# Performance work log

Measured on AMD Instinct MI355X. Metric: run time of the kernel, lower is better.

## Reference

```python
import jax, jax.numpy as jnp
import numpy as np

NUM_KNOTS = 64
HEAD_DIM = 4
SCALE = 0.5  # 1/sqrt(4)


def setup_inputs() -> dict:
    key = jax.random.key(0)
    ks = jax.random.split(key, 6)
    B, L, D = 4, 128, 256
    s = 1.0 / np.sqrt(D)
    return {
        "x": jax.random.normal(ks[0], (B, L, D), dtype=jnp.float32),
        "Wq": jax.random.normal(ks[1], (D, D), dtype=jnp.float32) * s,
        "Wk": jax.random.normal(ks[2], (D, D), dtype=jnp.float32) * s,
        "Wv": jax.random.normal(ks[3], (D, D), dtype=jnp.float32) * s,
        "Wo": jax.random.normal(ks[4], (D, D), dtype=jnp.float32) * s,
        "bo": jnp.zeros((D,), dtype=jnp.float32),
    }


def reference(x, Wq, Wk, Wv, Wo, bo):
    # x: [B, L, D], D = NUM_KNOTS * HEAD_DIM = 256
    B, L, D = x.shape
    N = L * NUM_KNOTS  # flattened 'knot' sequence length
    # nn.Linear applies x @ W.T
    q = (x @ Wq.T).reshape(B, N, HEAD_DIM)
    k = (x @ Wk.T).reshape(B, N, HEAD_DIM)
    v = (x @ Wv.T).reshape(B, N, HEAD_DIM)
    # full attention over the length-N knot sequence (head_dim = 4)
    logits = jnp.einsum("bnd,bmd->bnm", q, k) * SCALE  # [B, N, N]
    attn = jax.nn.softmax(logits, axis=-1)
    out = jnp.einsum("bnm,bmd->bnd", attn, v).reshape(B, L, D)
    return out @ Wo.T + bo
```

## Files before the change

### kernel.cpp

```cpp
#include <hip/hip_runtime.h>

#define NQ 8192
#define BLROWS 512
#define DIM 256

#define QSCALE 0.7213475204444817f

typedef float v2f __attribute__((ext_vector_type(2)));

__device__ __forceinline__ float ex2(float x) {
#if __has_builtin(__builtin_amdgcn_exp2f)
    return __builtin_amdgcn_exp2f(x);
#else
    return exp2f(x);
#endif
}

__device__ __forceinline__ void proj4_body(
    const float* __restrict__ A, const float* __restrict__ W,
    const float* __restrict__ bias, float* __restrict__ C,
    float scale, int rb)
{
    const int j = threadIdx.x;
    float acc[4] = {0.f, 0.f, 0.f, 0.f};
    const float4* __restrict__ W4 = reinterpret_cast<const float4*>(W + j * DIM);
    const float*  __restrict__ A0 = A + rb * DIM;

    #pragma unroll 4
    for (int d4 = 0; d4 < DIM / 4; ++d4) {
        const float4 w = W4[d4];
        #pragma unroll
        for (int r = 0; r < 4; ++r) {
            const float4 a = reinterpret_cast<const float4*>(A0 + r * DIM)[d4];
            acc[r] = fmaf(a.x, w.x, acc[r]);
            acc[r] = fmaf(a.y, w.y, acc[r]);
            acc[r] = fmaf(a.z, w.z, acc[r]);
            acc[r] = fmaf(a.w, w.w, acc[r]);
        }
    }
    const float b = bias ? bias[j] : 0.f;
    #pragma unroll
    for (int r = 0; r < 4; ++r)
        C[(rb + r) * DIM + j] = fmaf(acc[r], scale, b);
}

__global__ __launch_bounds__(256) void qkv_proj(
    const float* __restrict__ x,
    const float* __restrict__ Wq, const float* __restrict__ Wk,
    const float* __restrict__ Wv,
    float* __restrict__ Qb, float* __restrict__ Kb, float* __restrict__ Vb)
{
    const int m = blockIdx.y;
    const float* W = (m == 0) ? Wq : (m == 1) ? Wk : Wv;
    float* C       = (m == 0) ? Qb : (m == 1) ? Kb : Vb;
    const float sc = (m == 0) ? QSCALE : 1.0f;
    proj4_body(x, W, nullptr, C, sc, blockIdx.x * 4);
}

__global__ __launch_bounds__(256) void proj4_kernel(
    const float* __restrict__ A, const float* __restrict__ W,
    const float* __restrict__ bias, float* __restrict__ C, float scale)
{
    proj4_body(A, W, bias, C, scale, blockIdx.x * 4);
}

__global__ __launch_bounds__(256) void attn_partial(
    const float* __restrict__ Q, const float* __restrict__ K,
    const float* __restrict__ V, float* __restrict__ P)
{
    const int lane = threadIdx.x & 63;
    const int w    = __builtin_amdgcn_readfirstlane(threadIdx.x >> 6);
    const int qt   = blockIdx.x;
    const int ks   = blockIdx.y;
    const int b    = blockIdx.z;

    const float4* __restrict__ Qp = reinterpret_cast<const float4*>(Q) + b * NQ + qt * 256;
    const float4* __restrict__ Kp = reinterpret_cast<const float4*>(K) + b * NQ + ks * 1024 + w * 256;
    const float4* __restrict__ Vp = reinterpret_cast<const float4*>(V) + b * NQ + ks * 1024 + w * 256;

    v2f qx[2], qy[2], qz[2], qw[2];
    #pragma unroll
    for (int p = 0; p < 2; ++p) {
        const float4 t0 = Qp[(2 * p)     * 64 + lane];
        const float4 t1 = Qp[(2 * p + 1) * 64 + lane];
        qx[p] = v2f{t0.x, t1.x};
        qy[p] = v2f{t0.y, t1.y};
        qz[p] = v2f{t0.z, t1.z};
        qw[p] = v2f{t0.w, t1.w};
    }
    v2f a0[2], a1[2], a2[2], a3[2], ls[2];
    #pragma unroll
    for (int p = 0; p < 2; ++p) {
        a0[p] = v2f{0.f, 0.f}; a1[p] = v2f{0.f, 0.f};
        a2[p] = v2f{0.f, 0.f}; a3[p] = v2f{0.f, 0.f};
        ls[p] = v2f{0.f, 0.f};
    }

    #pragma unroll 8
    for (int j = 0; j < 256; ++j) {
        const float4 k4 = Kp[j];
        const float4 v4 = Vp[j];
        #pragma unroll
        for (int p = 0; p < 2; ++p) {
            v2f s = qx[p] * k4.x;
            s = __builtin_elementwise_fma(qy[p], v2f{k4.y, k4.y}, s);
            s = __builtin_elementwise_fma(qz[p], v2f{k4.z, k4.z}, s);
            s = __builtin_elementwise_fma(qw[p], v2f{k4.w, k4.w}, s);
            const v2f e = v2f{ex2(s[0]), ex2(s[1])};
            ls[p] += e;
            a0[p] = __builtin_elementwise_fma(e, v2f{v4.x, v4.x}, a0[p]);
            a1[p] = __builtin_elementwise_fma(e, v2f{v4.y, v4.y}, a1[p]);
            a2[p] = __builtin_elementwise_fma(e, v2f{v4.z, v4.z}, a2[p]);
            a3[p] = __builtin_elementwise_fma(e, v2f{v4.w, v4.w}, a3[p]);
        }
    }

    __shared__ float red[4][256][5];
    #pragma unroll
    for (int p = 0; p < 2; ++p) {
        #pragma unroll
        for (int e = 0; e < 2; ++e) {
            float* pr = &red[w][(2 * p + e) * 64 + lane][0];
            pr[0] = ls[p][e]; pr[1] = a0[p][e]; pr[2] = a1[p][e];
            pr[3] = a2[p][e]; pr[4] = a3[p][e];
        }
    }
    __syncthreads();

    float* __restrict__ Pb = P + (size_t)((b * 8 + ks) * 5) * NQ + qt * 256;
    const int qq = threadIdx.x;
    #pragma unroll
    for (int c = 0; c < 5; ++c) {
        const float sred = red[0][qq][c] + red[1][qq][c] + red[2][qq][c] + red[3][qq][c];
        Pb[c * NQ + qq] = sred;
    }
}

__global__ __launch_bounds__(256) void attn_merge(
    const float* __restrict__ P, float* __restrict__ AO)
{
    const int idx = blockIdx.x * 256 + threadIdx.x;
    const int b = idx >> 13;
    const int n = idx & (NQ - 1);
    float l = 0.f, x0 = 0.f, x1 = 0.f, x2 = 0.f, x3 = 0.f;
    #pragma unroll
    for (int s = 0; s < 8; ++s) {
        const float* Pb = P + (size_t)((b * 8 + s) * 5) * NQ + n;
        l  += Pb[0];
        x0 += Pb[NQ];
        x1 += Pb[2 * NQ];
        x2 += Pb[3 * NQ];
        x3 += Pb[4 * NQ];
    }
    const float inv = 1.0f / l;
    reinterpret_cast<float4*>(AO)[idx] = make_float4(x0 * inv, x1 * inv, x2 * inv, x3 * inv);
}

extern "C" void kernel_launch(void* const* d_in, const int* in_sizes, int n_in,
                              void* d_out, int out_size, void* d_ws, size_t ws_size,
                              hipStream_t stream) {
    const float* x  = (const float*)d_in[0];
    const float* Wq = (const float*)d_in[1];
    const float* Wk = (const float*)d_in[2];
    const float* Wv = (const float*)d_in[3];
    const float* Wo = (const float*)d_in[4];
    const float* bo = (const float*)d_in[5];
    float* out = (float*)d_out;

    float* Qb = (float*)d_ws;
    float* Kb = Qb + BLROWS * DIM;
    float* Vb = Kb + BLROWS * DIM;
    float* AO = Vb + BLROWS * DIM;
    float* P  = AO + BLROWS * DIM;

    qkv_proj<<<dim3(128, 3), 256, 0, stream>>>(x, Wq, Wk, Wv, Qb, Kb, Vb);
    attn_partial<<<dim3(32, 8, 4), 256, 0, stream>>>(Qb, Kb, Vb, P);
    attn_merge<<<128, 256, 0, stream>>>(P, AO);
    proj4_kernel<<<128, 256, 0, stream>>>(AO, Wo, bo, out, 1.0f);
}
```

Baseline: 91.94 us.

## Double key-split slices and fuse softmax merge into output projection

```diff
diff --git a/kernel.cpp b/kernel.cpp
--- a/kernel.cpp
+++ b/kernel.cpp
@@ -3,6 +3,7 @@
 #define NQ 8192
 #define BLROWS 512
 #define DIM 256
+#define KSLICES 16
 
 #define QSCALE 0.7213475204444817f
 
@@ -16,15 +17,22 @@
 #endif
 }
 
-__device__ __forceinline__ void proj4_body(
-    const float* __restrict__ A, const float* __restrict__ W,
-    const float* __restrict__ bias, float* __restrict__ C,
-    float scale, int rb)
+__global__ __launch_bounds__(256) void qkv_proj(
+    const float* __restrict__ x,
+    const float* __restrict__ Wq, const float* __restrict__ Wk,
+    const float* __restrict__ Wv,
+    float* __restrict__ Qb, float* __restrict__ Kb, float* __restrict__ Vb)
 {
-    const int j = threadIdx.x;
+    const int m = blockIdx.y;
+    const float* W = (m == 0) ? Wq : (m == 1) ? Wk : Wv;
+    float* C       = (m == 0) ? Qb : (m == 1) ? Kb : Vb;
+    const float sc = (m == 0) ? QSCALE : 1.0f;
+    const int j  = threadIdx.x;
+    const int rb = blockIdx.x * 4;
+
     float acc[4] = {0.f, 0.f, 0.f, 0.f};
     const float4* __restrict__ W4 = reinterpret_cast<const float4*>(W + j * DIM);
-    const float*  __restrict__ A0 = A + rb * DIM;
+    const float*  __restrict__ A0 = x + rb * DIM;
 
     #pragma unroll 4
     for (int d4 = 0; d4 < DIM / 4; ++d4) {
@@ -38,30 +46,9 @@
             acc[r] = fmaf(a.w, w.w, acc[r]);
         }
     }
-    const float b = bias ? bias[j] : 0.f;
     #pragma unroll
     for (int r = 0; r < 4; ++r)
-        C[(rb + r) * DIM + j] = fmaf(acc[r], scale, b);
-}
-
-__global__ __launch_bounds__(256) void qkv_proj(
-    const float* __restrict__ x,
-    const float* __restrict__ Wq, const float* __restrict__ Wk,
-    const float* __restrict__ Wv,
-    float* __restrict__ Qb, float* __restrict__ Kb, float* __restrict__ Vb)
-{
-    const int m = blockIdx.y;
-    const float* W = (m == 0) ? Wq : (m == 1) ? Wk : Wv;
-    float* C       = (m == 0) ? Qb : (m == 1) ? Kb : Vb;
-    const float sc = (m == 0) ? QSCALE : 1.0f;
-    proj4_body(x, W, nullptr, C, sc, blockIdx.x * 4);
-}
-
-__global__ __launch_bounds__(256) void proj4_kernel(
-    const float* __restrict__ A, const float* __restrict__ W,
-    const float* __restrict__ bias, float* __restrict__ C, float scale)
-{
-    proj4_body(A, W, bias, C, scale, blockIdx.x * 4);
+        C[(rb + r) * DIM + j] = acc[r] * sc;
 }
 
 __global__ __launch_bounds__(256) void attn_partial(
@@ -75,8 +62,8 @@
     const int b    = blockIdx.z;
 
     const float4* __restrict__ Qp = reinterpret_cast<const float4*>(Q) + b * NQ + qt * 256;
-    const float4* __restrict__ Kp = reinterpret_cast<const float4*>(K) + b * NQ + ks * 1024 + w * 256;
-    const float4* __restrict__ Vp = reinterpret_cast<const float4*>(V) + b * NQ + ks * 1024 + w * 256;
+    const float4* __restrict__ Kp = reinterpret_cast<const float4*>(K) + b * NQ + ks * 512 + w * 128;
+    const float4* __restrict__ Vp = reinterpret_cast<const float4*>(V) + b * NQ + ks * 512 + w * 128;
 
     v2f qx[2], qy[2], qz[2], qw[2];
     #pragma unroll
@@ -97,7 +84,7 @@
     }
 
     #pragma unroll 8
-    for (int j = 0; j < 256; ++j) {
+    for (int j = 0; j < 128; ++j) {
         const float4 k4 = Kp[j];
         const float4 v4 = Vp[j];
         #pragma unroll
@@ -127,7 +114,7 @@
     }
     __syncthreads();
 
-    float* __restrict__ Pb = P + (size_t)((b * 8 + ks) * 5) * NQ + qt * 256;
+    float* __restrict__ Pb = P + (size_t)((b * KSLICES + ks) * 5) * NQ + qt * 256;
     const int qq = threadIdx.x;
     #pragma unroll
     for (int c = 0; c < 5; ++c) {
@@ -136,24 +123,55 @@
     }
 }
 
-__global__ __launch_bounds__(256) void attn_merge(
-    const float* __restrict__ P, float* __restrict__ AO)
+__global__ __launch_bounds__(256) void merge_oproj(
+    const float* __restrict__ P, const float* __restrict__ Wo,
+    const float* __restrict__ bo, float* __restrict__ out)
 {
-    const int idx = blockIdx.x * 256 + threadIdx.x;
-    const int b = idx >> 13;
-    const int n = idx & (NQ - 1);
-    float l = 0.f, x0 = 0.f, x1 = 0.f, x2 = 0.f, x3 = 0.f;
+    __shared__ float aoL[4][DIM];
+
+    const int rb = blockIdx.x * 4;
+    const int b  = rb >> 7;
+    const int n0 = (rb & 127) * 64;
+    const int t  = threadIdx.x;
+
+    {
+        float sums[5] = {0.f, 0.f, 0.f, 0.f, 0.f};
+        const float* __restrict__ Pb = P + (size_t)(b * KSLICES * 5) * NQ + n0 + t;
+        #pragma unroll
+        for (int s = 0; s < KSLICES; ++s) {
+            #pragma unroll
+            for (int c = 0; c < 5; ++c)
+                sums[c] += Pb[(s * 5 + c) * NQ];
+        }
+        const float inv = 1.0f / sums[0];
+        const int row = t >> 6;
+        const int d0  = (t & 63) * 4;
+        aoL[row][d0 + 0] = sums[1] * inv;
+        aoL[row][d0 + 1] = sums[2] * inv;
+        aoL[row][d0 + 2] = sums[3] * inv;
+        aoL[row][d0 + 3] = sums[4] * inv;
+    }
+    __syncthreads();
+
+    const int j = t;
+    float acc[4] = {0.f, 0.f, 0.f, 0.f};
+    const float4* __restrict__ W4 = reinterpret_cast<const float4*>(Wo + j * DIM);
+    #pragma unroll 4
+    for (int d4 = 0; d4 < DIM / 4; ++d4) {
+        const float4 wv = W4[d4];
+        #pragma unroll
+        for (int r = 0; r < 4; ++r) {
+            const float4 a = reinterpret_cast<const float4*>(&aoL[r][0])[d4];
+            acc[r] = fmaf(a.x, wv.x, acc[r]);
+            acc[r] = fmaf(a.y, wv.y, acc[r]);
+            acc[r] = fmaf(a.z, wv.z, acc[r]);
+            acc[r] = fmaf(a.w, wv.w, acc[r]);
+        }
+    }
+    const float bias = bo[j];
     #pragma unroll
-    for (int s = 0; s < 8; ++s) {
-        const float* Pb = P + (size_t)((b * 8 + s) * 5) * NQ + n;
-        l  += Pb[0];
-        x0 += Pb[NQ];
-        x1 += Pb[2 * NQ];
-        x2 += Pb[3 * NQ];
-        x3 += Pb[4 * NQ];
-    }
-    const float inv = 1.0f / l;
-    reinterpret_cast<float4*>(AO)[idx] = make_float4(x0 * inv, x1 * inv, x2 * inv, x3 * inv);
+    for (int r = 0; r < 4; ++r)
+        out[(rb + r) * DIM + j] = acc[r] + bias;
 }
 
 extern "C" void kernel_launch(void* const* d_in, const int* in_sizes, int n_in,
@@ -170,11 +188,9 @@
     float* Qb = (float*)d_ws;
     float* Kb = Qb + BLROWS * DIM;
     float* Vb = Kb + BLROWS * DIM;
-    float* AO = Vb + BLROWS * DIM;
-    float* P  = AO + BLROWS * DIM;
+    float* P  = Vb + BLROWS * DIM;
 
     qkv_proj<<<dim3(128, 3), 256, 0, stream>>>(x, Wq, Wk, Wv, Qb, Kb, Vb);
-    attn_partial<<<dim3(32, 8, 4), 256, 0, stream>>>(Qb, Kb, Vb, P);
-    attn_merge<<<128, 256, 0, stream>>>(P, AO);
-    proj4_kernel<<<128, 256, 0, stream>>>(AO, Wo, bo, out, 1.0f);
+    attn_partial<<<dim3(32, KSLICES, 4), 256, 0, stream>>>(Qb, Kb, Vb, P);
+    merge_oproj<<<128, 256, 0, stream>>>(P, Wo, bo, out);
 }
```

After: 86.90 us. 5.5% less time.
